# Kernel tuning notes

Measured on AMD Instinct MI355X. Metric: run time of the kernel, lower is better.

## Reference

```python
import jax, jax.numpy as jnp
import numpy as np

N_NODES = 50000
N_EDGES = 800000
NODE_IN = 256
EDGE_IN = 64
HEADS = 4
OUT = 64
NEG_SLOPE = 0.2  # dgl GATConv default


def setup_inputs() -> dict:
    key = jax.random.key(0)
    ks = jax.random.split(key, 10)
    node_feats = jax.random.normal(ks[0], (N_NODES, NODE_IN), dtype=jnp.float32)
    edge_feats = jax.random.normal(ks[1], (N_EDGES, EDGE_IN), dtype=jnp.float32)
    src = jax.random.randint(ks[2], (N_EDGES,), 0, N_NODES, dtype=jnp.int32)
    dst = jax.random.randint(ks[3], (N_EDGES,), 0, N_NODES, dtype=jnp.int32)
    # learned params (Xavier-ish scaling)
    W = jax.random.normal(ks[4], (NODE_IN, HEADS * OUT), dtype=jnp.float32) / np.sqrt(NODE_IN)
    We = jax.random.normal(ks[5], (EDGE_IN, HEADS * OUT), dtype=jnp.float32) / np.sqrt(EDGE_IN)
    attn_l = jax.random.normal(ks[6], (HEADS, OUT), dtype=jnp.float32) / np.sqrt(OUT)
    attn_r = jax.random.normal(ks[7], (HEADS, OUT), dtype=jnp.float32) / np.sqrt(OUT)
    attn_e = jax.random.normal(ks[8], (HEADS, OUT), dtype=jnp.float32) / np.sqrt(OUT)
    return {"node_feats": node_feats, "edge_feats": edge_feats, "W": W, "We": We,
            "attn_l": attn_l, "attn_r": attn_r, "attn_e": attn_e, "src": src, "dst": dst}


def reference(node_feats, edge_feats, W, We, attn_l, attn_r, attn_e, src, dst):
    # GAT with edge features (dropout disabled for deterministic reference).
    N = node_feats.shape[0]
    H, D = attn_l.shape
    h = (node_feats @ W).reshape(N, H, D)              # [N,H,D] projected nodes
    fe = (edge_feats @ We).reshape(-1, H, D)           # [E,H,D] projected edges
    el = jnp.sum(h * attn_l, axis=-1)                  # [N,H]
    er = jnp.sum(h * attn_r, axis=-1)                  # [N,H]
    ee = jnp.sum(fe * attn_e, axis=-1)                 # [E,H]
    e = jax.nn.leaky_relu(el[src] + er[dst] + ee, NEG_SLOPE)  # [E,H]
    # numerically stable segment softmax over incoming edges of each dst node
    emax = jax.ops.segment_max(e, dst, num_segments=N)         # [N,H]
    emax = jnp.where(jnp.isfinite(emax), emax, 0.0)            # empty segments -> 0
    ex = jnp.exp(e - emax[dst])                                # [E,H]
    denom = jax.ops.segment_sum(ex, dst, num_segments=N)       # [N,H]
    alpha = ex / (denom[dst] + 1e-9)                           # [E,H]
    out = jax.ops.segment_sum(alpha[..., None] * h[src], dst, num_segments=N)  # [N,H,D]
    return out
```

## Files before the change

### kernel.cpp

```cpp
#include <hip/hip_runtime.h>
#include <hip/hip_bf16.h>
#include <math.h>

#define N_NODES 50000
#define N_EDGES 800000
#define HEADS 4
#define HD 256
#define NEG_SLOPE 0.2f

typedef __attribute__((ext_vector_type(8))) short bf16x8;
typedef __attribute__((ext_vector_type(4))) float f32x4;

struct __align__(32) EPack {
    float ex[4];
    int   s;
    int   pad[3];
};

__device__ unsigned short g_Hb[N_NODES * HD];
__device__ float    g_el[N_NODES * HEADS];
__device__ float    g_er[N_NODES * HEADS];
__device__ EPack    g_ep[N_EDGES];
__device__ int      g_deg[N_NODES];
__device__ int      g_rowptr[N_NODES + 1];
__device__ int      g_cursor[N_NODES];
__device__ int      g_bsum[256];
__device__ float    g_Wea[64 * HEADS];
__device__ unsigned short g_Wbt[256 * 256];
__device__ unsigned short g_Wlrb[16 * 256];

__device__ __forceinline__ unsigned short f2bf(float f) {
    unsigned u = __float_as_uint(f);
    u += 0x7fffu + ((u >> 16) & 1u);
    return (unsigned short)(u >> 16);
}
__device__ __forceinline__ float bf_lo(unsigned u) {
    return __uint_as_float(u << 16);
}
__device__ __forceinline__ float bf_hi(unsigned u) {
    return __uint_as_float(u & 0xFFFF0000u);
}

__global__ void k_zero() {
    int g = blockIdx.x * 256 + threadIdx.x;
    if (g < N_NODES) g_deg[g] = 0;
}

__global__ void k_prep(const float* __restrict__ W, const float* __restrict__ We,
                       const float* __restrict__ al, const float* __restrict__ ar,
                       const float* __restrict__ ae, const int* __restrict__ dst) {
    int t = blockIdx.x * 256 + threadIdx.x;
    if (t < 256) {
        int k = t >> 2, h = t & 3;
        float s = 0.f;
        for (int d = 0; d < 64; ++d) s += We[k * 256 + h * 64 + d] * ae[h * 64 + d];
        g_Wea[t] = s;
    }
    if (t < 4096) {
        int c = t >> 8, k = t & 255;
        float s = 0.f;
        if (c < 4) {
            for (int d = 0; d < 64; ++d) s += W[k * 256 + c * 64 + d] * al[c * 64 + d];
        } else if (c < 8) {
            int h = c - 4;
            for (int d = 0; d < 64; ++d) s += W[k * 256 + h * 64 + d] * ar[h * 64 + d];
        }
        g_Wlrb[c * 256 + k] = f2bf(s);
    }
    for (int i = t; i < 65536; i += 50176) {
        int n = i >> 8, k = i & 255;
        g_Wbt[n * 256 + k] = f2bf(W[k * 256 + n]);
    }
    for (int e = t; e < N_EDGES; e += 50176)
        atomicAdd(&g_deg[dst[e]], 1);
}

#define BM 128
#define BK 32
__global__ __launch_bounds__(256) void k_gemm_mfma(const float* __restrict__ X) {
    __shared__ unsigned short As[BM][40];
    const int tid = threadIdx.x;
    const int wave = tid >> 6, lane = tid & 63;
    const int l15 = lane & 15, lg = lane >> 4;
    const int row0 = blockIdx.x * BM;

    f32x4 acc[8][4];
    f32x4 accE[8];
    #pragma unroll
    for (int i = 0; i < 8; ++i) {
        accE[i] = (f32x4){0.f, 0.f, 0.f, 0.f};
        #pragma unroll
        for (int j = 0; j < 4; ++j) acc[i][j] = (f32x4){0.f, 0.f, 0.f, 0.f};
    }

    for (int k0 = 0; k0 < 256; k0 += BK) {
        #pragma unroll
        for (int q = 0; q < 4; ++q) {
            int f = q * 256 + tid;
            int r = f >> 3;
            int kq = (f & 7) << 2;
            int grow = row0 + r;
            float4 v = make_float4(0.f, 0.f, 0.f, 0.f);
            if (grow < N_NODES) v = *(const float4*)(X + grow * 256 + k0 + kq);
            ushort4 b;
            b.x = f2bf(v.x); b.y = f2bf(v.y); b.z = f2bf(v.z); b.w = f2bf(v.w);
            *(ushort4*)&As[r][kq] = b;
        }
        bf16x8 bfr[4];
        #pragma unroll
        for (int nf = 0; nf < 4; ++nf) {
            int n = wave * 64 + nf * 16 + l15;
            bfr[nf] = *(const bf16x8*)(g_Wbt + n * 256 + k0 + lg * 8);
        }
        bf16x8 bfrE = *(const bf16x8*)(g_Wlrb + l15 * 256 + k0 + lg * 8);
        __syncthreads();
        #pragma unroll
        for (int mf = 0; mf < 8; ++mf) {
            bf16x8 afr = *(const bf16x8*)&As[mf * 16 + l15][lg * 8];
            #pragma unroll
            for (int nf = 0; nf < 4; ++nf)
                acc[mf][nf] = __builtin_amdgcn_mfma_f32_16x16x32_bf16(
                    afr, bfr[nf], acc[mf][nf], 0, 0, 0);
            accE[mf] = __builtin_amdgcn_mfma_f32_16x16x32_bf16(
                afr, bfrE, accE[mf], 0, 0, 0);
        }
        __syncthreads();
    }
    #pragma unroll
    for (int mf = 0; mf < 8; ++mf) {
        #pragma unroll
        for (int r = 0; r < 4; ++r) {
            int grow = row0 + mf * 16 + lg * 4 + r;
            if (grow < N_NODES) {
                #pragma unroll
                for (int nf = 0; nf < 4; ++nf) {
                    int col = wave * 64 + nf * 16 + l15;
                    g_Hb[grow * 256 + col] = f2bf(acc[mf][nf][r]);
                }
                if (wave == 0) {
                    if (l15 < 4) g_el[grow * 4 + l15] = accE[mf][r];
                    else if (l15 < 8) g_er[grow * 4 + (l15 - 4)] = accE[mf][r];
                }
            }
        }
    }
}

__global__ void k_scan1() {
    __shared__ int s[256];
    int tid = threadIdx.x;
    int g = blockIdx.x * 256 + tid;
    int v = (g < N_NODES) ? g_deg[g] : 0;
    s[tid] = v; __syncthreads();
    for (int o = 1; o < 256; o <<= 1) {
        int t = (tid >= o) ? s[tid - o] : 0;
        __syncthreads();
        s[tid] += t;
        __syncthreads();
    }
    if (g < N_NODES) g_rowptr[g] = s[tid] - v;
    if (tid == 255) g_bsum[blockIdx.x] = s[255];
}

__global__ void k_scan2(int nb) {
    __shared__ int s[256];
    int tid = threadIdx.x;
    int v = (tid < nb) ? g_bsum[tid] : 0;
    s[tid] = v; __syncthreads();
    for (int o = 1; o < 256; o <<= 1) {
        int t = (tid >= o) ? s[tid - o] : 0;
        __syncthreads();
        s[tid] += t;
        __syncthreads();
    }
    if (tid < nb) g_bsum[tid] = s[tid] - v;
}

__global__ void k_scan3() {
    int g = blockIdx.x * 256 + threadIdx.x;
    if (g < N_NODES) {
        int r = g_rowptr[g] + g_bsum[blockIdx.x];
        g_rowptr[g] = r;
        g_cursor[g] = r;
    }
    if (g == 0) g_rowptr[N_NODES] = N_EDGES;
}

__global__ __launch_bounds__(256) void k_edge(const float* __restrict__ EF,
                                              const int* __restrict__ src,
                                              const int* __restrict__ dst) {
    __shared__ float sEF[32][258];
    __shared__ float4 sW[64];
    const int tid = threadIdx.x;
    if (tid < 64) sW[tid] = *(const float4*)(g_Wea + tid * 4);
    const int e0 = blockIdx.x * 256;

    float p0 = 0.f, p1 = 0.f, p2 = 0.f, p3 = 0.f;
    #pragma unroll
    for (int kc = 0; kc < 2; ++kc) {
        __syncthreads();
        #pragma unroll
        for (int q = 0; q < 8; ++q) {
            int f = q * 256 + tid;
            int e = f >> 3;
            int c = (f & 7) << 2;
            float4 v = *(const float4*)(EF + (size_t)(e0 + e) * 64 + kc * 32 + c);
            sEF[c + 0][e] = v.x; sEF[c + 1][e] = v.y;
            sEF[c + 2][e] = v.z; sEF[c + 3][e] = v.w;
        }
        __syncthreads();
        #pragma unroll
        for (int k = 0; k < 32; ++k) {
            float x = sEF[k][tid];
            float4 w = sW[kc * 32 + k];
            p0 += x * w.x; p1 += x * w.y; p2 += x * w.z; p3 += x * w.w;
        }
    }
    const int eid = e0 + tid;
    const int s = src[eid], d = dst[eid];
    float4 l4 = *(const float4*)(g_el + s * 4);
    float4 r4 = *(const float4*)(g_er + d * 4);
    float e0v = p0 + l4.x + r4.x;
    float e1v = p1 + l4.y + r4.y;
    float e2v = p2 + l4.z + r4.z;
    float e3v = p3 + l4.w + r4.w;
    e0v = e0v > 0.f ? e0v : NEG_SLOPE * e0v;
    e1v = e1v > 0.f ? e1v : NEG_SLOPE * e1v;
    e2v = e2v > 0.f ? e2v : NEG_SLOPE * e2v;
    e3v = e3v > 0.f ? e3v : NEG_SLOPE * e3v;
    int p = atomicAdd(&g_cursor[d], 1);
    *(float4*)g_ep[p].ex =
        make_float4(__expf(e0v), __expf(e1v), __expf(e2v), __expf(e3v));
    g_ep[p].s = s;
}

__global__ __launch_bounds__(256) void k_agg(float* __restrict__ out) {
    int node = (blockIdx.x * 256 + threadIdx.x) >> 6;
    int lane = threadIdx.x & 63;
    if (node >= N_NODES) return;
    int start = g_rowptr[node], end = g_rowptr[node + 1];
    int myh = lane >> 4, sub = lane & 15;
    const int hoff = myh * 64 + sub * 4;

    float den = 0.f;
    float a0 = 0.f, a1 = 0.f, a2 = 0.f, a3 = 0.f;
    #pragma unroll 8
    for (int i = start; i < end; ++i) {
        float ex = g_ep[i].ex[myh];
        int s = g_ep[i].s;
        uint2 hv = *(const uint2*)(g_Hb + s * 256 + hoff);
        den += ex;
        a0 += ex * bf_lo(hv.x); a1 += ex * bf_hi(hv.x);
        a2 += ex * bf_lo(hv.y); a3 += ex * bf_hi(hv.y);
    }
    float rden = 1.0f / (den + 1e-9f);
    *(float4*)(out + node * 256 + lane * 4) =
        make_float4(a0 * rden, a1 * rden, a2 * rden, a3 * rden);
}

extern "C" void kernel_launch(void* const* d_in, const int* in_sizes, int n_in,
                              void* d_out, int out_size, void* d_ws, size_t ws_size,
                              hipStream_t stream) {
    const float* X  = (const float*)d_in[0];
    const float* EF = (const float*)d_in[1];
    const float* W  = (const float*)d_in[2];
    const float* We = (const float*)d_in[3];
    const float* al = (const float*)d_in[4];
    const float* ar = (const float*)d_in[5];
    const float* ae = (const float*)d_in[6];
    const int* src  = (const int*)d_in[7];
    const int* dst  = (const int*)d_in[8];
    float* out = (float*)d_out;

    const int nb_scan = (N_NODES + 255) / 256;

    k_zero<<<nb_scan, 256, 0, stream>>>();
    k_prep<<<nb_scan, 256, 0, stream>>>(W, We, al, ar, ae, dst);
    k_gemm_mfma<<<(N_NODES + BM - 1) / BM, 256, 0, stream>>>(X);
    k_scan1<<<nb_scan, 256, 0, stream>>>();
    k_scan2<<<1, 256, 0, stream>>>(nb_scan);
    k_scan3<<<nb_scan, 256, 0, stream>>>();
    k_edge<<<N_EDGES / 256, 256, 0, stream>>>(EF, src, dst);
    k_agg<<<(N_NODES + 3) / 4, 256, 0, stream>>>(out);
}
```

Measured before the change: 257.3 us.

## Split node GEMM across two column slabs and double the K tile

The node-projection GEMM now launches a 2D grid so that each block computes only 128 of the 256 output columns. This doubles the block count from about 391 to 782 for better CU occupancy and halves the accumulator registers. The K tile grows from 32 to 64 to halve the number of loop iterations and barriers. The cost is that each X row tile is loaded and converted to bf16 twice (once per slab), and the attention-logit MFMA work runs only in slab 0, which unbalances the two slabs.

```diff
diff --git a/kernel.cpp b/kernel.cpp
--- a/kernel.cpp
+++ b/kernel.cpp
@@ -76,29 +76,30 @@
 }
 
 #define BM 128
-#define BK 32
+#define BK 64
 __global__ __launch_bounds__(256) void k_gemm_mfma(const float* __restrict__ X) {
-    __shared__ unsigned short As[BM][40];
+    __shared__ unsigned short As[BM][BK + 8];
     const int tid = threadIdx.x;
     const int wave = tid >> 6, lane = tid & 63;
     const int l15 = lane & 15, lg = lane >> 4;
     const int row0 = blockIdx.x * BM;
-
-    f32x4 acc[8][4];
+    const int slab = blockIdx.y;
+
+    f32x4 acc[8][2];
     f32x4 accE[8];
     #pragma unroll
     for (int i = 0; i < 8; ++i) {
         accE[i] = (f32x4){0.f, 0.f, 0.f, 0.f};
         #pragma unroll
-        for (int j = 0; j < 4; ++j) acc[i][j] = (f32x4){0.f, 0.f, 0.f, 0.f};
+        for (int j = 0; j < 2; ++j) acc[i][j] = (f32x4){0.f, 0.f, 0.f, 0.f};
     }
 
     for (int k0 = 0; k0 < 256; k0 += BK) {
         #pragma unroll
-        for (int q = 0; q < 4; ++q) {
+        for (int q = 0; q < 8; ++q) {
             int f = q * 256 + tid;
-            int r = f >> 3;
-            int kq = (f & 7) << 2;
+            int r = f >> 4;
+            int kq = (f & 15) << 2;
             int grow = row0 + r;
             float4 v = make_float4(0.f, 0.f, 0.f, 0.f);
             if (grow < N_NODES) v = *(const float4*)(X + grow * 256 + k0 + kq);
@@ -106,23 +107,30 @@
             b.x = f2bf(v.x); b.y = f2bf(v.y); b.z = f2bf(v.z); b.w = f2bf(v.w);
             *(ushort4*)&As[r][kq] = b;
         }
-        bf16x8 bfr[4];
-        #pragma unroll
-        for (int nf = 0; nf < 4; ++nf) {
-            int n = wave * 64 + nf * 16 + l15;
-            bfr[nf] = *(const bf16x8*)(g_Wbt + n * 256 + k0 + lg * 8);
-        }
-        bf16x8 bfrE = *(const bf16x8*)(g_Wlrb + l15 * 256 + k0 + lg * 8);
-        __syncthreads();
-        #pragma unroll
-        for (int mf = 0; mf < 8; ++mf) {
-            bf16x8 afr = *(const bf16x8*)&As[mf * 16 + l15][lg * 8];
+        bf16x8 bfr[2][2], bfrE[2];
+        #pragma unroll
+        for (int kk = 0; kk < 2; ++kk) {
             #pragma unroll
-            for (int nf = 0; nf < 4; ++nf)
-                acc[mf][nf] = __builtin_amdgcn_mfma_f32_16x16x32_bf16(
-                    afr, bfr[nf], acc[mf][nf], 0, 0, 0);
-            accE[mf] = __builtin_amdgcn_mfma_f32_16x16x32_bf16(
-                afr, bfrE, accE[mf], 0, 0, 0);
+            for (int nf = 0; nf < 2; ++nf) {
+                int n = slab * 128 + wave * 32 + nf * 16 + l15;
+                bfr[kk][nf] = *(const bf16x8*)(g_Wbt + n * 256 + k0 + kk * 32 + lg * 8);
+            }
+            bfrE[kk] = *(const bf16x8*)(g_Wlrb + l15 * 256 + k0 + kk * 32 + lg * 8);
+        }
+        __syncthreads();
+        #pragma unroll
+        for (int kk = 0; kk < 2; ++kk) {
+            #pragma unroll
+            for (int mf = 0; mf < 8; ++mf) {
+                bf16x8 afr = *(const bf16x8*)&As[mf * 16 + l15][kk * 32 + lg * 8];
+                #pragma unroll
+                for (int nf = 0; nf < 2; ++nf)
+                    acc[mf][nf] = __builtin_amdgcn_mfma_f32_16x16x32_bf16(
+                        afr, bfr[kk][nf], acc[mf][nf], 0, 0, 0);
+                if (slab == 0)
+                    accE[mf] = __builtin_amdgcn_mfma_f32_16x16x32_bf16(
+                        afr, bfrE[kk], accE[mf], 0, 0, 0);
+            }
         }
         __syncthreads();
     }
@@ -133,11 +141,11 @@
             int grow = row0 + mf * 16 + lg * 4 + r;
             if (grow < N_NODES) {
                 #pragma unroll
-                for (int nf = 0; nf < 4; ++nf) {
-                    int col = wave * 64 + nf * 16 + l15;
+                for (int nf = 0; nf < 2; ++nf) {
+                    int col = slab * 128 + wave * 32 + nf * 16 + l15;
                     g_Hb[grow * 256 + col] = f2bf(acc[mf][nf][r]);
                 }
-                if (wave == 0) {
+                if (slab == 0 && wave == 0) {
                     if (l15 < 4) g_el[grow * 4 + l15] = accE[mf][r];
                     else if (l15 < 8) g_er[grow * 4 + (l15 - 4)] = accE[mf][r];
                 }
@@ -276,7 +284,7 @@
 
     k_zero<<<nb_scan, 256, 0, stream>>>();
     k_prep<<<nb_scan, 256, 0, stream>>>(W, We, al, ar, ae, dst);
-    k_gemm_mfma<<<(N_NODES + BM - 1) / BM, 256, 0, stream>>>(X);
+    k_gemm_mfma<<<dim3((N_NODES + BM - 1) / BM, 2), 256, 0, stream>>>(X);
     k_scan1<<<nb_scan, 256, 0, stream>>>();
     k_scan2<<<1, 256, 0, stream>>>(nb_scan);
     k_scan3<<<nb_scan, 256, 0, stream>>>();
```

Result: faster. 247.1 us (-3.9%).
